# Kernel tuning notes

Measured on AMD Instinct MI355X. Metric: run time of the kernel, lower is better.

## Reference

```python
import jax, jax.numpy as jnp
import numpy as np

B, S, D = 4, 2048, 1024
H, HK = 16, 4          # num_heads, num_heads_kv
HD = D // H            # head_dim = 64
G = H // HK            # kv groups = 4


def setup_inputs() -> dict:
    key = jax.random.key(0)
    ks = jax.random.split(key, 7)
    s = 0.02
    return {
        "query": jax.random.normal(ks[0], (B, S, D), jnp.float32),
        "key":   jax.random.normal(ks[1], (B, S, D), jnp.float32),
        "value": jax.random.normal(ks[2], (B, S, D), jnp.float32),
        # weights stored (in, out); equivalent to torch Linear y = x @ W.T
        "Wq": jax.random.normal(ks[3], (D, H * HD), jnp.float32) * s,
        "Wk": jax.random.normal(ks[4], (D, HK * HD), jnp.float32) * s,
        "Wv": jax.random.normal(ks[5], (D, HK * HD), jnp.float32) * s,
        "Wo": jax.random.normal(ks[6], (H * HD, D), jnp.float32) * s,
    }


def reference(query, key, value, Wq, Wk, Wv, Wo):
    b, qlen, _ = query.shape
    kvlen = key.shape[1]
    # projections
    q = (query @ Wq).reshape(b, qlen, H, HD)        # [b,q,H,hd]
    k = (key @ Wk).reshape(b, kvlen, HK, HD)        # [b,s,HK,hd]
    v = (value @ Wv).reshape(b, kvlen, HK, HD)      # [b,s,HK,hd]
    # GQA: q head h attends kv head h//G (repeat_interleave semantics)
    qg = q.reshape(b, qlen, HK, G, HD)              # head = kv*G + group
    scale = 1.0 / jnp.sqrt(jnp.asarray(HD, q.dtype))
    # scores [b,HK,G,q,s] -- broadcast kv heads, no materialized repeat
    scores = jnp.einsum('bqkgd,bskd->bkgqs', qg, k) * scale
    attn = jax.nn.softmax(scores, axis=-1)
    out = jnp.einsum('bkgqs,bskd->bqkgd', attn, v)  # [b,q,HK,G,hd]
    out = out.reshape(b, qlen, H * HD)
    return out @ Wo
```

## Files before the change

### kernel.cpp

```cpp
#include <hip/hip_runtime.h>


typedef unsigned short u16;
typedef unsigned int   u32;
typedef __bf16 bf16x4 __attribute__((ext_vector_type(4)));
typedef __bf16 bf16x8 __attribute__((ext_vector_type(8)));
typedef float  f32x4  __attribute__((ext_vector_type(4)));

#define MFMA(a,b,c) __builtin_amdgcn_mfma_f32_16x16x32_bf16((a),(b),(c),0,0,0)

#define GLDS(g, l) __builtin_amdgcn_global_load_lds(                          \
    (const __attribute__((address_space(1))) void*)(g),                       \
    (__attribute__((address_space(3))) void*)(l), 16, 0, 0)

#if __has_builtin(__builtin_amdgcn_exp2f)
#define EXP2(x) __builtin_amdgcn_exp2f(x)
#else
#define EXP2(x) exp2f(x)
#endif

__device__ __forceinline__ u16 f2bf(float f){
    u32 u = __builtin_bit_cast(u32, f);
    u += 0x7fffu + ((u >> 16) & 1u);
    return (u16)(u >> 16);
}
__device__ __forceinline__ u32 pk2(float a, float b){
#if __has_builtin(__builtin_amdgcn_cvt_pk_bf16_f32)
    auto r = __builtin_amdgcn_cvt_pk_bf16_f32(a, b);
    return __builtin_bit_cast(u32, r);
#else
    return (u32)f2bf(a) | ((u32)f2bf(b) << 16);
#endif
}
__device__ __forceinline__ bf16x8 ldfrag(const u16* p){
    return *(const bf16x8*)p;
}
__device__ __forceinline__ bf16x8 ld2x64(const u16* p){
    bf16x4 lo = *(const bf16x4*)p;
    bf16x4 hi = *(const bf16x4*)(p + 4);
    bf16x8 r;
    r[0]=lo[0]; r[1]=lo[1]; r[2]=lo[2]; r[3]=lo[3];
    r[4]=hi[0]; r[5]=hi[1]; r[6]=hi[2]; r[7]=hi[3];
    return r;
}

__global__ __launch_bounds__(256) void prep(const float* __restrict__ Wq,
                                            const float* __restrict__ Wk,
                                            const float* __restrict__ Wv,
                                            const float* __restrict__ Wo,
                                            u16* WqT, u16* WkT, u16* WvT, u16* WoT){
    const int tid = threadIdx.x, bid = blockIdx.x;
    __shared__ float T[32][33];
    const float* W; u16* WT; int N, i;
    if (bid < 1024)      { W = Wq; WT = WqT; N = 1024; i = bid; }
    else if (bid < 1280) { W = Wk; WT = WkT; N =  256; i = bid - 1024; }
    else if (bid < 1536) { W = Wv; WT = WvT; N =  256; i = bid - 1280; }
    else                 { W = Wo; WT = WoT; N = 1024; i = bid - 1536; }
    int kt = (i & 31) * 32, nt = (i >> 5) * 32;
    int r = tid >> 3, c = tid & 7;
    float4 vv = *(const float4*)(W + (size_t)(kt + r) * N + nt + c * 4);
    T[r][c*4+0] = vv.x; T[r][c*4+1] = vv.y; T[r][c*4+2] = vv.z; T[r][c*4+3] = vv.w;
    __syncthreads();
    u32 lo = pk2(T[c*4+0][r], T[c*4+1][r]);
    u32 hi = pk2(T[c*4+2][r], T[c*4+3][r]);
    *(uint2*)(WT + (size_t)(nt + r) * 1024 + kt + c * 4) = make_uint2(lo, hi);
}

template<int ATYPE, int EPI>
__device__ __forceinline__ void gemm_body(const void* __restrict__ Ap,
                                          const u16* __restrict__ Bt,
                                          void* __restrict__ Cp,
                                          int N, int K, int m0, int n0,
                                          u16* As, u16* Bs, float oscale){
    const int tid  = threadIdx.x;
    const int wave = tid >> 6, lane = tid & 63;
    const int quad = lane >> 4, l15 = lane & 15;
    const int wm = wave >> 1, wn = wave & 1;
    const int srow = lane >> 3;
    const int scol = ((lane & 7) ^ srow) * 8;
    const int swz  = l15 & 7;
    const int c4 = tid & 15, r0 = tid >> 4;

    f32x4 acc[4][4];
    #pragma unroll
    for (int i = 0; i < 4; ++i)
        #pragma unroll
        for (int j = 0; j < 4; ++j) acc[i][j] = (f32x4){0.f, 0.f, 0.f, 0.f};

    const int nkt = K >> 6;
    float4 areg[8];

    auto loadA = [&](int kt){
        const float* A = (const float*)Ap;
        #pragma unroll
        for (int p = 0; p < 8; ++p)
            areg[p] = *(const float4*)(A + (size_t)(m0 + r0 + p*16) * K
                                         + kt*64 + c4*4);
    };
    auto writeA = [&](){
        #pragma unroll
        for (int p = 0; p < 8; ++p){
            int r = r0 + p*16;
            *(uint2*)&As[r*64 + (((c4>>1) ^ (r&7))*8 + (c4&1)*4)] =
                make_uint2(pk2(areg[p].x, areg[p].y), pk2(areg[p].z, areg[p].w));
        }
    };

    if constexpr (ATYPE == 0) loadA(0);

    for (int kt = 0; kt < nkt; ++kt){
        if (kt) __syncthreads();
        if constexpr (ATYPE == 0){
            writeA();
            if (kt + 1 < nkt) loadA(kt + 1);
        } else {
            const u16* A = (const u16*)Ap;
            const u16* ga = A + (size_t)(m0 + wave*32 + srow) * K + kt*64 + scol;
            u16* la = As + (wave*32) * 64;
            #pragma unroll
            for (int p = 0; p < 4; ++p)
                GLDS(ga + (size_t)(p*8) * K, la + p*8*64);
        }
        {
            const u16* gb = Bt + (size_t)(n0 + wave*32 + srow) * K + kt*64 + scol;
            u16* lb = Bs + (wave*32) * 64;
            #pragma unroll
            for (int p = 0; p < 4; ++p)
                GLDS(gb + (size_t)(p*8) * K, lb + p*8*64);
        }
        __syncthreads();
        #pragma unroll
        for (int ks = 0; ks < 2; ++ks){
            bf16x8 af[4], bfr[4];
            #pragma unroll
            for (int mt = 0; mt < 4; ++mt)
                af[mt] = ldfrag(&As[(wm*64 + mt*16 + l15) * 64 +
                                    (((ks*4 + quad) ^ swz) * 8)]);
            #pragma unroll
            for (int nt = 0; nt < 4; ++nt)
                bfr[nt] = ldfrag(&Bs[(wn*64 + nt*16 + l15) * 64 +
                                     (((ks*4 + quad) ^ swz) * 8)]);
            #pragma unroll
            for (int mt = 0; mt < 4; ++mt)
                #pragma unroll
                for (int nt = 0; nt < 4; ++nt){
                    if constexpr (EPI == 1)
                        acc[mt][nt] = MFMA(af[mt], bfr[nt], acc[mt][nt]);
                    else
                        acc[mt][nt] = MFMA(bfr[nt], af[mt], acc[mt][nt]);
                }
        }
    }
    #pragma unroll
    for (int mt = 0; mt < 4; ++mt){
        #pragma unroll
        for (int nt = 0; nt < 4; ++nt){
            if constexpr (EPI == 1){
                int rowb = m0 + wm*64 + mt*16 + quad*4;
                int col  = n0 + wn*64 + nt*16 + l15;
                u16* C = (u16*)Cp;
                int bb = rowb >> 11, s = rowb & 2047;
                u32 lo = pk2(acc[mt][nt][0], acc[mt][nt][1]);
                u32 hi = pk2(acc[mt][nt][2], acc[mt][nt][3]);
                *(uint2*)(C + (size_t)(bb * 256 + col) * 2048 + s) = make_uint2(lo, hi);
            } else {
                int row  = m0 + wm*64 + mt*16 + l15;
                int colb = n0 + wn*64 + nt*16 + quad*4;
                if constexpr (EPI == 0){
                    u16* C = (u16*)Cp;
                    u32 lo = pk2(acc[mt][nt][0]*oscale, acc[mt][nt][1]*oscale);
                    u32 hi = pk2(acc[mt][nt][2]*oscale, acc[mt][nt][3]*oscale);
                    *(uint2*)(C + (size_t)row * N + colb) = make_uint2(lo, hi);
                } else {
                    float* C = (float*)Cp;
                    *(f32x4*)(C + (size_t)row * N + colb) = acc[mt][nt];
                }
            }
        }
    }
}

__global__ __launch_bounds__(256, 4) void gemm_qkv(const float* q, const u16* WqT, u16* Qp,
                                                   const float* k, const u16* WkT, u16* Kp,
                                                   const float* v, const u16* WvT, u16* Vt,
                                                   float qscale){
    __shared__ u16 As[128 * 64];
    __shared__ u16 Bs[128 * 64];
    int bid = blockIdx.x;
    if (bid < 512){
        int x = bid & 7, s = bid >> 3;
        int m = x * 8 + (s >> 3), n = s & 7;
        gemm_body<0,0>((const void*)q, WqT, (void*)Qp, 1024, 1024,
                       m * 128, n * 128, As, Bs, qscale);
    } else if (bid < 640){
        int i = bid - 512;
        int x = i & 7, s = i >> 3;
        int m = x * 8 + (s >> 1), n = s & 1;
        gemm_body<0,0>((const void*)k, WkT, (void*)Kp, 256, 1024,
                       m * 128, n * 128, As, Bs, 1.0f);
    } else {
        int i = bid - 640;
        int x = i & 7, s = i >> 3;
        int m = x * 8 + (s >> 1), n = s & 1;
        gemm_body<0,1>((const void*)v, WvT, (void*)Vt, 256, 1024,
                       m * 128, n * 128, As, Bs, 1.0f);
    }
}

__global__ __launch_bounds__(256, 4) void gemm_o(const u16* AO, const u16* WoT,
                                                 float* Out){
    __shared__ u16 As[128 * 64];
    __shared__ u16 Bs[128 * 64];
    int bid = blockIdx.x;
    int x = bid & 7, s = bid >> 3;
    int m = x * 8 + (s >> 3), n = s & 7;
    gemm_body<1,2>((const void*)AO, WoT, (void*)Out, 1024, 1024,
                   m * 128, n * 128, As, Bs, 1.0f);
}

__global__ __launch_bounds__(512, 4) void attn_k(const u16* __restrict__ Qp,
                                                 const u16* __restrict__ Kp,
                                                 const u16* __restrict__ Vt,
                                                 u16* __restrict__ AO){
    constexpr int S = 2048, Dm = 1024, NKV = 256, PST = 68;
    __shared__ u16 Kb[2][64 * 64];
    __shared__ u16 Vb[2][64 * 64];
    __shared__ u16 Ps[256 * PST];
    const int tid = threadIdx.x, wave = tid >> 6, lane = tid & 63;
    const int quad = lane >> 4, l15 = lane & 15;
    const int h = blockIdx.y, b = blockIdx.z;
    const int hk = h >> 2, q0 = blockIdx.x * 256;
    u16* pw = Ps + wave * (32 * PST);

    const int srow = lane >> 3;
    const int scol = ((lane & 7) ^ srow) * 8;
    const int swz  = l15 & 7;

    auto issue = [&](int t){
        int j0 = t * 64, bufi = t & 1;
        int r = wave * 8 + srow;
        GLDS(Kp + (size_t)(b * S + j0 + r) * NKV + hk * 64 + scol,
             &Kb[bufi][wave * 8 * 64]);
        GLDS(Vt + (size_t)(b * NKV + hk * 64 + r) * S + j0 + scol,
             &Vb[bufi][wave * 8 * 64]);
    };

    issue(0);
    {
        int c8 = tid & 7, r0 = tid >> 3;
        #pragma unroll
        for (int p = 0; p < 4; ++p){
            int r = r0 + p * 64;
            uint4 v = *(const uint4*)(Qp + (size_t)(b * S + q0 + r) * Dm + h * 64 + c8 * 8);
            *(uint2*)&Ps[r * PST + c8 * 8]     = make_uint2(v.x, v.y);
            *(uint2*)&Ps[r * PST + c8 * 8 + 4] = make_uint2(v.z, v.w);
        }
    }
    __syncthreads();
    bf16x8 qf[2][2];
    #pragma unroll
    for (int mt = 0; mt < 2; ++mt)
        #pragma unroll
        for (int ks = 0; ks < 2; ++ks)
            qf[mt][ks] = ld2x64(&Ps[(wave*32 + mt*16 + l15) * PST + ks*32 + quad*8]);

    const u32 one2 = 0x3F803F80u;
    const bf16x8 ones = __builtin_bit_cast(bf16x8, make_uint4(one2, one2, one2, one2));

    f32x4 O[4][2];
    #pragma unroll
    for (int dt = 0; dt < 4; ++dt)
        #pragma unroll
        for (int mt = 0; mt < 2; ++mt) O[dt][mt] = (f32x4){0.f, 0.f, 0.f, 0.f};
    f32x4 sums[2];
    #pragma unroll
    for (int mt = 0; mt < 2; ++mt) sums[mt] = (f32x4){0.f, 0.f, 0.f, 0.f};

    for (int t = 0; t < 32; ++t){
        __syncthreads();
        if (t < 31) issue(t + 1);
        const u16* Kt = Kb[t & 1];
        const u16* Vs = Vb[t & 1];
        f32x4 sf[2][4];
        #pragma unroll
        for (int mt = 0; mt < 2; ++mt)
            #pragma unroll
            for (int nt = 0; nt < 4; ++nt) sf[mt][nt] = (f32x4){0.f, 0.f, 0.f, 0.f};
        #pragma unroll
        for (int ks = 0; ks < 2; ++ks){
            bf16x8 ak[4];
            #pragma unroll
            for (int nt = 0; nt < 4; ++nt)
                ak[nt] = ldfrag(&Kt[(nt*16 + l15) * 64 + (((ks*4 + quad) ^ swz) * 8)]);
            #pragma unroll
            for (int mt = 0; mt < 2; ++mt)
                #pragma unroll
                for (int nt = 0; nt < 4; ++nt)
                    sf[mt][nt] = MFMA(ak[nt], qf[mt][ks], sf[mt][nt]);
        }
        #pragma unroll
        for (int mt = 0; mt < 2; ++mt)
            #pragma unroll
            for (int nt = 0; nt < 4; ++nt){
                float e0 = EXP2(sf[mt][nt][0]);
                float e1 = EXP2(sf[mt][nt][1]);
                float e2 = EXP2(sf[mt][nt][2]);
                float e3 = EXP2(sf[mt][nt][3]);
                *(uint2*)&pw[(mt*16 + l15) * PST + nt*16 + quad*4] =
                    make_uint2(pk2(e0, e1), pk2(e2, e3));
            }
        __threadfence_block();
        #pragma unroll
        for (int ks = 0; ks < 2; ++ks){
            bf16x8 av[4], bp[2];
            #pragma unroll
            for (int dt = 0; dt < 4; ++dt)
                av[dt] = ldfrag(&Vs[(dt*16 + l15) * 64 + (((ks*4 + quad) ^ swz) * 8)]);
            #pragma unroll
            for (int mt = 0; mt < 2; ++mt)
                bp[mt] = ld2x64(&pw[(mt*16 + l15) * PST + ks*32 + quad*8]);
            #pragma unroll
            for (int mt = 0; mt < 2; ++mt)
                sums[mt] = MFMA(ones, bp[mt], sums[mt]);
            #pragma unroll
            for (int dt = 0; dt < 4; ++dt)
                #pragma unroll
                for (int mt = 0; mt < 2; ++mt)
                    O[dt][mt] = MFMA(av[dt], bp[mt], O[dt][mt]);
        }
    }
    #pragma unroll
    for (int mt = 0; mt < 2; ++mt){
        float inv = 1.0f / sums[mt][0];
        size_t row = (size_t)(b * S + q0 + wave*32 + mt*16 + l15);
        #pragma unroll
        for (int dt = 0; dt < 4; ++dt){
            u32 lo = pk2(O[dt][mt][0] * inv, O[dt][mt][1] * inv);
            u32 hi = pk2(O[dt][mt][2] * inv, O[dt][mt][3] * inv);
            *(uint2*)(AO + row * Dm + h * 64 + dt*16 + quad*4) = make_uint2(lo, hi);
        }
    }
}

extern "C" void kernel_launch(void* const* d_in, const int* in_sizes, int n_in,
                              void* d_out, int out_size, void* d_ws, size_t ws_size,
                              hipStream_t stream){
    const float* q  = (const float*)d_in[0];
    const float* k  = (const float*)d_in[1];
    const float* v  = (const float*)d_in[2];
    const float* Wq = (const float*)d_in[3];
    const float* Wk = (const float*)d_in[4];
    const float* Wv = (const float*)d_in[5];
    const float* Wo = (const float*)d_in[6];
    char* ws = (char*)d_ws;
    const size_t MB = 1u << 20;
    u16* WqT = (u16*)(ws);
    u16* WkT = (u16*)(ws + 2*MB);
    u16* WvT = (u16*)(ws + 2*MB + 512*1024);
    u16* WoT = (u16*)(ws + 3*MB);
    u16* Qp  = (u16*)(ws + 5*MB);
    u16* Kp  = (u16*)(ws + 21*MB);
    u16* Vt  = (u16*)(ws + 25*MB);
    u16* AO  = (u16*)(ws + 29*MB);

    const float cexp = 0.125f * 1.44269504f;

    prep<<<dim3(2560), 256, 0, stream>>>(Wq, Wk, Wv, Wo, WqT, WkT, WvT, WoT);
    gemm_qkv<<<dim3(768), 256, 0, stream>>>(q, WqT, Qp, k, WkT, Kp,
                                            v, WvT, Vt, cexp);
    attn_k<<<dim3(8, 16, 4), 512, 0, stream>>>(Qp, Kp, Vt, AO);
    gemm_o<<<dim3(512), 256, 0, stream>>>(AO, WoT, (float*)d_out);
}
```

Before: 326.0 us.

## Double-buffer GEMM LDS tiles with explicit waitcnt-controlled prefetch pipeline

Restructures the shared GEMM body into a two-stage software pipeline with ping-pong LDS buffers for A and B. The next K tile is prefetched while MFMAs run on the current one, with manual s_waitcnt and sched_barrier controlling ordering. The aim is to hide global-load latency behind compute in the QKV and output projection GEMMs. LDS use per block doubles and the launch-bounds occupancy hint is dropped, so fewer blocks may fit per CU, and the hand-tuned vmcnt values must match the exact number of outstanding loads.

```diff
diff --git a/kernel.cpp b/kernel.cpp
--- a/kernel.cpp
+++ b/kernel.cpp
@@ -12,6 +12,11 @@
 #define GLDS(g, l) __builtin_amdgcn_global_load_lds(                          \
     (const __attribute__((address_space(1))) void*)(g),                       \
     (__attribute__((address_space(3))) void*)(l), 16, 0, 0)
+
+#define SBAR()   __builtin_amdgcn_s_barrier()
+#define SCHED0() __builtin_amdgcn_sched_barrier(0)
+#define WAITV(n) asm volatile("s_waitcnt vmcnt(" #n ")" ::: "memory")
+#define WAITL()  asm volatile("s_waitcnt lgkmcnt(0)" ::: "memory")
 
 #if __has_builtin(__builtin_amdgcn_exp2f)
 #define EXP2(x) __builtin_amdgcn_exp2f(x)
@@ -72,6 +77,7 @@
                                           void* __restrict__ Cp,
                                           int N, int K, int m0, int n0,
                                           u16* As, u16* Bs, float oscale){
+    constexpr int TSZ = 128 * 64;
     const int tid  = threadIdx.x;
     const int wave = tid >> 6, lane = tid & 63;
     const int quad = lane >> 4, l15 = lane & 15;
@@ -88,58 +94,54 @@
         for (int j = 0; j < 4; ++j) acc[i][j] = (f32x4){0.f, 0.f, 0.f, 0.f};
 
     const int nkt = K >> 6;
-    float4 areg[8];
-
-    auto loadA = [&](int kt){
-        const float* A = (const float*)Ap;
-        #pragma unroll
-        for (int p = 0; p < 8; ++p)
-            areg[p] = *(const float4*)(A + (size_t)(m0 + r0 + p*16) * K
-                                         + kt*64 + c4*4);
-    };
-    auto writeA = [&](){
+    float4 aregA[8], aregB[8];
+
+    auto loadA = [&](int kt, float4* dst){
+        if (kt < nkt){
+            const float* A = (const float*)Ap;
+            #pragma unroll
+            for (int p = 0; p < 8; ++p)
+                dst[p] = *(const float4*)(A + (size_t)(m0 + r0 + p*16) * K
+                                            + kt*64 + c4*4);
+        }
+    };
+    auto writeA = [&](const float4* src, u16* dstLds){
         #pragma unroll
         for (int p = 0; p < 8; ++p){
             int r = r0 + p*16;
-            *(uint2*)&As[r*64 + (((c4>>1) ^ (r&7))*8 + (c4&1)*4)] =
-                make_uint2(pk2(areg[p].x, areg[p].y), pk2(areg[p].z, areg[p].w));
-        }
-    };
-
-    if constexpr (ATYPE == 0) loadA(0);
-
-    for (int kt = 0; kt < nkt; ++kt){
-        if (kt) __syncthreads();
-        if constexpr (ATYPE == 0){
-            writeA();
-            if (kt + 1 < nkt) loadA(kt + 1);
-        } else {
+            *(uint2*)&dstLds[r*64 + (((c4>>1) ^ (r&7))*8 + (c4&1)*4)] =
+                make_uint2(pk2(src[p].x, src[p].y), pk2(src[p].z, src[p].w));
+        }
+    };
+    auto issueAg = [&](int kt, u16* la){
+        if (kt < nkt){
             const u16* A = (const u16*)Ap;
             const u16* ga = A + (size_t)(m0 + wave*32 + srow) * K + kt*64 + scol;
-            u16* la = As + (wave*32) * 64;
             #pragma unroll
             for (int p = 0; p < 4; ++p)
-                GLDS(ga + (size_t)(p*8) * K, la + p*8*64);
-        }
-        {
+                GLDS(ga + (size_t)(p*8) * K, la + (wave*32)*64 + p*8*64);
+        }
+    };
+    auto issueB = [&](int kt, u16* lb){
+        if (kt < nkt){
             const u16* gb = Bt + (size_t)(n0 + wave*32 + srow) * K + kt*64 + scol;
-            u16* lb = Bs + (wave*32) * 64;
             #pragma unroll
             for (int p = 0; p < 4; ++p)
-                GLDS(gb + (size_t)(p*8) * K, lb + p*8*64);
-        }
-        __syncthreads();
+                GLDS(gb + (size_t)(p*8) * K, lb + (wave*32)*64 + p*8*64);
+        }
+    };
+    auto mfmaPhase = [&](const u16* Asc, const u16* Bsc){
         #pragma unroll
         for (int ks = 0; ks < 2; ++ks){
             bf16x8 af[4], bfr[4];
             #pragma unroll
             for (int mt = 0; mt < 4; ++mt)
-                af[mt] = ldfrag(&As[(wm*64 + mt*16 + l15) * 64 +
-                                    (((ks*4 + quad) ^ swz) * 8)]);
+                af[mt] = ldfrag(&Asc[(wm*64 + mt*16 + l15) * 64 +
+                                     (((ks*4 + quad) ^ swz) * 8)]);
             #pragma unroll
             for (int nt = 0; nt < 4; ++nt)
-                bfr[nt] = ldfrag(&Bs[(wn*64 + nt*16 + l15) * 64 +
-                                     (((ks*4 + quad) ^ swz) * 8)]);
+                bfr[nt] = ldfrag(&Bsc[(wn*64 + nt*16 + l15) * 64 +
+                                      (((ks*4 + quad) ^ swz) * 8)]);
             #pragma unroll
             for (int mt = 0; mt < 4; ++mt)
                 #pragma unroll
@@ -150,7 +152,57 @@
                         acc[mt][nt] = MFMA(bfr[nt], af[mt], acc[mt][nt]);
                 }
         }
-    }
+    };
+
+    if constexpr (ATYPE == 0){
+        loadA(0, aregA);
+        issueB(0, Bs);
+        loadA(1, aregB);
+        WAITV(12); SCHED0();
+        writeA(aregA, As);
+        WAITL(); SCHED0();
+    } else {
+        issueAg(0, As);
+        issueB(0, Bs);
+    }
+
+    for (int t = 0; t < nkt; t += 2){
+        SBAR(); SCHED0();
+        issueB(t+1, Bs + TSZ);
+        if constexpr (ATYPE == 0){
+            loadA(t+2, aregA);
+            if (t+2 < nkt)      { WAITV(12); }
+            else if (t+1 < nkt) { WAITV(4);  }
+            else                { WAITV(0);  }
+            SCHED0();
+            if (t+1 < nkt) writeA(aregB, As + TSZ);
+            WAITL(); SCHED0();
+        } else {
+            issueAg(t+1, As + TSZ);
+            if (t+1 < nkt) { WAITV(8); } else { WAITV(0); }
+            SCHED0();
+        }
+        SBAR(); SCHED0();
+        mfmaPhase(As, Bs);
+        SBAR(); SCHED0();
+        issueB(t+2, Bs);
+        if constexpr (ATYPE == 0){
+            loadA(t+3, aregB);
+            if (t+3 < nkt)      { WAITV(12); }
+            else if (t+2 < nkt) { WAITV(4);  }
+            else                { WAITV(0);  }
+            SCHED0();
+            if (t+2 < nkt) writeA(aregA, As);
+            WAITL(); SCHED0();
+        } else {
+            issueAg(t+2, As);
+            if (t+2 < nkt) { WAITV(8); } else { WAITV(0); }
+            SCHED0();
+        }
+        SBAR(); SCHED0();
+        mfmaPhase(As + TSZ, Bs + TSZ);
+    }
+
     #pragma unroll
     for (int mt = 0; mt < 4; ++mt){
         #pragma unroll
@@ -180,12 +232,12 @@
     }
 }
 
-__global__ __launch_bounds__(256, 4) void gemm_qkv(const float* q, const u16* WqT, u16* Qp,
-                                                   const float* k, const u16* WkT, u16* Kp,
-                                                   const float* v, const u16* WvT, u16* Vt,
-                                                   float qscale){
-    __shared__ u16 As[128 * 64];
-    __shared__ u16 Bs[128 * 64];
+__global__ __launch_bounds__(256) void gemm_qkv(const float* q, const u16* WqT, u16* Qp,
+                                                const float* k, const u16* WkT, u16* Kp,
+                                                const float* v, const u16* WvT, u16* Vt,
+                                                float qscale){
+    __shared__ u16 As[2 * 128 * 64];
+    __shared__ u16 Bs[2 * 128 * 64];
     int bid = blockIdx.x;
     if (bid < 512){
         int x = bid & 7, s = bid >> 3;
@@ -207,10 +259,10 @@
     }
 }
 
-__global__ __launch_bounds__(256, 4) void gemm_o(const u16* AO, const u16* WoT,
-                                                 float* Out){
-    __shared__ u16 As[128 * 64];
-    __shared__ u16 Bs[128 * 64];
+__global__ __launch_bounds__(256) void gemm_o(const u16* AO, const u16* WoT,
+                                              float* Out){
+    __shared__ u16 As[2 * 128 * 64];
+    __shared__ u16 Bs[2 * 128 * 64];
     int bid = blockIdx.x;
     int x = bid & 7, s = bid >> 3;
     int m = x * 8 + (s >> 3), n = s & 7;
```

After: 319.5 us. 2.0% less time.

## Double-buffer GEMM LDS tiles and use 512-thread blocks with smaller per-wave tiles

Applied to the files above, without the earlier changes.

The projection GEMMs now keep two LDS buffers and prefetch the next K-tile (global-to-LDS loads for bf16 operands, register loads for fp32 A) while MFMAs run on the current tile, which removes one barrier per iteration. Block size doubles to 512 threads, so each wave now computes 32x64 instead of 64x64, cutting accumulator registers and raising parallelism. LDS use per block doubles to 64KB, which may limit how many blocks fit per CU, and each wave reuses fewer fragments.

```diff
diff --git a/kernel.cpp b/kernel.cpp
--- a/kernel.cpp
+++ b/kernel.cpp
@@ -72,6 +72,7 @@
                                           void* __restrict__ Cp,
                                           int N, int K, int m0, int n0,
                                           u16* As, u16* Bs, float oscale){
+    constexpr int TSZ = 128 * 64;
     const int tid  = threadIdx.x;
     const int wave = tid >> 6, lane = tid & 63;
     const int quad = lane >> 4, l15 = lane & 15;
@@ -81,67 +82,57 @@
     const int swz  = l15 & 7;
     const int c4 = tid & 15, r0 = tid >> 4;
 
-    f32x4 acc[4][4];
-    #pragma unroll
-    for (int i = 0; i < 4; ++i)
+    f32x4 acc[2][4];
+    #pragma unroll
+    for (int i = 0; i < 2; ++i)
         #pragma unroll
         for (int j = 0; j < 4; ++j) acc[i][j] = (f32x4){0.f, 0.f, 0.f, 0.f};
 
     const int nkt = K >> 6;
-    float4 areg[8];
+    float4 areg[4];
 
     auto loadA = [&](int kt){
         const float* A = (const float*)Ap;
         #pragma unroll
-        for (int p = 0; p < 8; ++p)
-            areg[p] = *(const float4*)(A + (size_t)(m0 + r0 + p*16) * K
+        for (int p = 0; p < 4; ++p)
+            areg[p] = *(const float4*)(A + (size_t)(m0 + r0 + p*32) * K
                                          + kt*64 + c4*4);
     };
-    auto writeA = [&](){
-        #pragma unroll
-        for (int p = 0; p < 8; ++p){
-            int r = r0 + p*16;
-            *(uint2*)&As[r*64 + (((c4>>1) ^ (r&7))*8 + (c4&1)*4)] =
+    auto writeA = [&](u16* dst){
+        #pragma unroll
+        for (int p = 0; p < 4; ++p){
+            int r = r0 + p*32;
+            *(uint2*)&dst[r*64 + (((c4>>1) ^ (r&7))*8 + (c4&1)*4)] =
                 make_uint2(pk2(areg[p].x, areg[p].y), pk2(areg[p].z, areg[p].w));
         }
     };
-
-    if constexpr (ATYPE == 0) loadA(0);
-
-    for (int kt = 0; kt < nkt; ++kt){
-        if (kt) __syncthreads();
-        if constexpr (ATYPE == 0){
-            writeA();
-            if (kt + 1 < nkt) loadA(kt + 1);
-        } else {
-            const u16* A = (const u16*)Ap;
-            const u16* ga = A + (size_t)(m0 + wave*32 + srow) * K + kt*64 + scol;
-            u16* la = As + (wave*32) * 64;
-            #pragma unroll
-            for (int p = 0; p < 4; ++p)
-                GLDS(ga + (size_t)(p*8) * K, la + p*8*64);
-        }
-        {
-            const u16* gb = Bt + (size_t)(n0 + wave*32 + srow) * K + kt*64 + scol;
-            u16* lb = Bs + (wave*32) * 64;
-            #pragma unroll
-            for (int p = 0; p < 4; ++p)
-                GLDS(gb + (size_t)(p*8) * K, lb + p*8*64);
-        }
-        __syncthreads();
+    auto issueAg = [&](int kt, u16* la){
+        const u16* A = (const u16*)Ap;
+        const u16* ga = A + (size_t)(m0 + wave*16 + srow) * K + kt*64 + scol;
+        #pragma unroll
+        for (int p = 0; p < 2; ++p)
+            GLDS(ga + (size_t)(p*8) * K, la + (wave*16 + p*8) * 64);
+    };
+    auto issueB = [&](int kt, u16* lb){
+        const u16* gb = Bt + (size_t)(n0 + wave*16 + srow) * K + kt*64 + scol;
+        #pragma unroll
+        for (int p = 0; p < 2; ++p)
+            GLDS(gb + (size_t)(p*8) * K, lb + (wave*16 + p*8) * 64);
+    };
+    auto mfmaPhase = [&](const u16* Asc, const u16* Bsc){
         #pragma unroll
         for (int ks = 0; ks < 2; ++ks){
-            bf16x8 af[4], bfr[4];
-            #pragma unroll
-            for (int mt = 0; mt < 4; ++mt)
-                af[mt] = ldfrag(&As[(wm*64 + mt*16 + l15) * 64 +
-                                    (((ks*4 + quad) ^ swz) * 8)]);
+            bf16x8 af[2], bfr[4];
+            #pragma unroll
+            for (int mt = 0; mt < 2; ++mt)
+                af[mt] = ldfrag(&Asc[(wm*32 + mt*16 + l15) * 64 +
+                                     (((ks*4 + quad) ^ swz) * 8)]);
             #pragma unroll
             for (int nt = 0; nt < 4; ++nt)
-                bfr[nt] = ldfrag(&Bs[(wn*64 + nt*16 + l15) * 64 +
-                                     (((ks*4 + quad) ^ swz) * 8)]);
-            #pragma unroll
-            for (int mt = 0; mt < 4; ++mt)
+                bfr[nt] = ldfrag(&Bsc[(wn*64 + nt*16 + l15) * 64 +
+                                      (((ks*4 + quad) ^ swz) * 8)]);
+            #pragma unroll
+            for (int mt = 0; mt < 2; ++mt)
                 #pragma unroll
                 for (int nt = 0; nt < 4; ++nt){
                     if constexpr (EPI == 1)
@@ -150,13 +141,42 @@
                         acc[mt][nt] = MFMA(bfr[nt], af[mt], acc[mt][nt]);
                 }
         }
-    }
-    #pragma unroll
-    for (int mt = 0; mt < 4; ++mt){
+    };
+
+    if constexpr (ATYPE == 0){
+        loadA(0);
+        issueB(0, Bs);
+        writeA(As);
+    } else {
+        issueAg(0, As);
+        issueB(0, Bs);
+    }
+    __syncthreads();
+
+    for (int t = 0; t < nkt; ++t){
+        u16* Asc = As + (t & 1) * TSZ;
+        u16* Bsc = Bs + (t & 1) * TSZ;
+        u16* Aso = As + ((t & 1) ^ 1) * TSZ;
+        u16* Bso = Bs + ((t & 1) ^ 1) * TSZ;
+        const bool more = (t + 1 < nkt);
+        if (more){
+            if constexpr (ATYPE == 0) loadA(t + 1);
+            else                      issueAg(t + 1, Aso);
+            issueB(t + 1, Bso);
+        }
+        mfmaPhase(Asc, Bsc);
+        if constexpr (ATYPE == 0){
+            if (more) writeA(Aso);
+        }
+        __syncthreads();
+    }
+
+    #pragma unroll
+    for (int mt = 0; mt < 2; ++mt){
         #pragma unroll
         for (int nt = 0; nt < 4; ++nt){
             if constexpr (EPI == 1){
-                int rowb = m0 + wm*64 + mt*16 + quad*4;
+                int rowb = m0 + wm*32 + mt*16 + quad*4;
                 int col  = n0 + wn*64 + nt*16 + l15;
                 u16* C = (u16*)Cp;
                 int bb = rowb >> 11, s = rowb & 2047;
@@ -164,7 +184,7 @@
                 u32 hi = pk2(acc[mt][nt][2], acc[mt][nt][3]);
                 *(uint2*)(C + (size_t)(bb * 256 + col) * 2048 + s) = make_uint2(lo, hi);
             } else {
-                int row  = m0 + wm*64 + mt*16 + l15;
+                int row  = m0 + wm*32 + mt*16 + l15;
                 int colb = n0 + wn*64 + nt*16 + quad*4;
                 if constexpr (EPI == 0){
                     u16* C = (u16*)Cp;
@@ -180,12 +200,12 @@
     }
 }
 
-__global__ __launch_bounds__(256, 4) void gemm_qkv(const float* q, const u16* WqT, u16* Qp,
+__global__ __launch_bounds__(512, 4) void gemm_qkv(const float* q, const u16* WqT, u16* Qp,
                                                    const float* k, const u16* WkT, u16* Kp,
                                                    const float* v, const u16* WvT, u16* Vt,
                                                    float qscale){
-    __shared__ u16 As[128 * 64];
-    __shared__ u16 Bs[128 * 64];
+    __shared__ u16 As[2 * 128 * 64];
+    __shared__ u16 Bs[2 * 128 * 64];
     int bid = blockIdx.x;
     if (bid < 512){
         int x = bid & 7, s = bid >> 3;
@@ -207,10 +227,10 @@
     }
 }
 
-__global__ __launch_bounds__(256, 4) void gemm_o(const u16* AO, const u16* WoT,
+__global__ __launch_bounds__(512, 4) void gemm_o(const u16* AO, const u16* WoT,
                                                  float* Out){
-    __shared__ u16 As[128 * 64];
-    __shared__ u16 Bs[128 * 64];
+    __shared__ u16 As[2 * 128 * 64];
+    __shared__ u16 Bs[2 * 128 * 64];
     int bid = blockIdx.x;
     int x = bid & 7, s = bid >> 3;
     int m = x * 8 + (s >> 3), n = s & 7;
@@ -366,8 +386,8 @@
     const float cexp = 0.125f * 1.44269504f;
 
     prep<<<dim3(2560), 256, 0, stream>>>(Wq, Wk, Wv, Wo, WqT, WkT, WvT, WoT);
-    gemm_qkv<<<dim3(768), 256, 0, stream>>>(q, WqT, Qp, k, WkT, Kp,
+    gemm_qkv<<<dim3(768), 512, 0, stream>>>(q, WqT, Qp, k, WkT, Kp,
                                             v, WvT, Vt, cexp);
     attn_k<<<dim3(8, 16, 4), 512, 0, stream>>>(Qp, Kp, Vt, AO);
-    gemm_o<<<dim3(512), 256, 0, stream>>>(AO, WoT, (float*)d_out);
-}
+    gemm_o<<<dim3(512), 512, 0, stream>>>(AO, WoT, (float*)d_out);
+}
```

Measured after the change: 301.7 us. -7.5%, faster.
